# Kernel optimization log

Hardware: AMD Instinct MI355X
Metric: run time of the kernel (lower is better)

Reference implementation:

```python
import jax, jax.numpy as jnp
import numpy as np

DIM = 512
HIDDEN = int(DIM * 0.2)  # 102
K_TOKENS = 64
N_TOKENS = 65536
LN_EPS = 1e-5


def setup_inputs() -> dict:
    key = jax.random.key(0)
    ks = jax.random.split(key, 8)
    x = jax.random.normal(ks[0], (N_TOKENS, DIM), dtype=jnp.float32)
    ln_gamma = jnp.ones((DIM,), dtype=jnp.float32)
    ln_beta = jnp.zeros((DIM,), dtype=jnp.float32)
    W1 = jax.random.normal(ks[1], (DIM, HIDDEN), dtype=jnp.float32) / np.sqrt(DIM)
    b1 = jnp.zeros((HIDDEN,), dtype=jnp.float32)
    W2 = jax.random.normal(ks[2], (HIDDEN, K_TOKENS), dtype=jnp.float32) / np.sqrt(HIDDEN)
    b2 = jnp.zeros((K_TOKENS,), dtype=jnp.float32)
    scale = jnp.ones((1, 1), dtype=jnp.float32)
    return {
        "x": x,
        "ln_gamma": ln_gamma,
        "ln_beta": ln_beta,
        "W1": W1,
        "b1": b1,
        "W2": W2,
        "b2": b2,
        "scale": scale,
        "keeped_tokens": K_TOKENS,
    }


def reference(x, ln_gamma, ln_beta, W1, b1, W2, b2, scale, keeped_tokens):
    # LayerNorm over last dim
    mu = jnp.mean(x, axis=-1, keepdims=True)
    var = jnp.mean(jnp.square(x - mu), axis=-1, keepdims=True)
    h = (x - mu) * jax.lax.rsqrt(var + LN_EPS) * ln_gamma + ln_beta
    # fc1 + exact GELU (torch default) + dynamic fc2 scorer
    h = jax.nn.gelu(h @ W1 + b1, approximate=False)  # [N, HIDDEN]
    w = h @ W2 + b2                                   # [N, K]
    # transpose, scale, softmax over tokens
    w = w.T * scale                                   # [K, N]
    w = jax.nn.softmax(w, axis=1)
    # weighted token aggregation
    return w @ x                                      # [K, DIM]
```

## Files before the change

### kernel.cpp

```cpp
#include <hip/hip_runtime.h>
#include <math.h>

#define N_TOK 65536
#define DIM   512
#define HID   102
#define KTOK  64
#define NTILE 4096
#define LN_EPS 1e-5f

typedef __attribute__((ext_vector_type(8))) short short8;
typedef __attribute__((ext_vector_type(4))) float f32x4;

#define WS_LOGITS 0u
#define WS_PART   4194304u
#define WS_PM     (WS_PART + 4194304u)
#define WS_PS     (WS_PM + 262144u)
#define WS_W1F    (WS_PS + 262144u)
#define WS_W2F    (WS_W1F + 32768u)
#define WS_UB     (WS_W2F + 4096u)
#define WS_VV     (WS_UB + 128u)
#define WS_SMAX   (WS_VV + 128u)
#define WS_SINV   (WS_SMAX + 64u)

__device__ __forceinline__ unsigned short f2bf(float f) {
    unsigned int u = __float_as_uint(f);
    unsigned int r = (u + 0x7fffu + ((u >> 16) & 1u)) >> 16;
    return (unsigned short)r;
}
__device__ __forceinline__ float bf2f(unsigned short h) {
    return __uint_as_float(((unsigned int)h) << 16);
}

__device__ __forceinline__ void gload_lds16(const void* g, void* l) {
    __builtin_amdgcn_global_load_lds(
        (const __attribute__((address_space(1))) unsigned int*)g,
        (__attribute__((address_space(3))) unsigned int*)l, 16, 0, 0);
}

__device__ __forceinline__ void bar_lds() {
    asm volatile("s_waitcnt lgkmcnt(0)" ::: "memory");
    __builtin_amdgcn_s_barrier();
    __builtin_amdgcn_sched_barrier(0);
}

__global__ __launch_bounds__(256) void prep_k(const float* __restrict__ W1,
                                              const float* __restrict__ gamma,
                                              const float* __restrict__ W2,
                                              unsigned short* __restrict__ W1f,
                                              unsigned short* __restrict__ W2f) {
    const int idx = blockIdx.x * 256 + threadIdx.x;
    {
        const int e = idx & 7, lane = (idx >> 3) & 63;
        const int jj = (idx >> 9) & 7, kc = (idx >> 12) & 15;
        const int j = jj * 16 + (lane & 15);
        const int d = kc * 32 + (lane >> 4) * 8 + e;
        W1f[idx] = (j < HID) ? f2bf(gamma[d] * W1[d * HID + j]) : (unsigned short)0;
    }
    if (idx < 8192) {
        const int e = idx & 7, lane = (idx >> 3) & 63;
        const int kc = (idx >> 9) & 3, N = (idx >> 11) & 3;
        const int j = kc * 32 + (lane >> 4) * 8 + e;
        const int k = N * 16 + (lane & 15);
        W2f[idx] = (j < HID) ? f2bf(W2[j * KTOK + k]) : (unsigned short)0;
    }
}

__global__ __launch_bounds__(512) void prep2_k(const float* __restrict__ W1,
                                               const float* __restrict__ b1,
                                               const float* __restrict__ gamma,
                                               const float* __restrict__ beta,
                                               float* __restrict__ ub,
                                               float* __restrict__ vv) {
    __shared__ float su[4][128], sv[4][128];
    const int t = threadIdx.x;
    const int j = t & 127, q = t >> 7;
    float u = 0.0f, v = 0.0f;
    if (j < HID) {
        #pragma unroll 8
        for (int d = q * 128; d < q * 128 + 128; ++d) {
            const float wv = W1[d * HID + j];
            u = fmaf(beta[d], wv, u);
            v = fmaf(gamma[d], wv, v);
        }
    }
    su[q][j] = u; sv[q][j] = v;
    __syncthreads();
    if (q == 0) {
        ub[j] = su[0][j] + su[1][j] + su[2][j] + su[3][j] +
                ((j < HID) ? b1[j] : 0.0f);
        vv[j] = sv[0][j] + sv[1][j] + sv[2][j] + sv[3][j];
    }
}

__global__ __launch_bounds__(512) void scorer_k(const float* __restrict__ x,
                                                const unsigned short* __restrict__ W1f,
                                                const unsigned short* __restrict__ W2f,
                                                const float* __restrict__ ub,
                                                const float* __restrict__ vv,
                                                const float* __restrict__ b2,
                                                const float* __restrict__ scale,
                                                float* __restrict__ logits,
                                                float* __restrict__ pm,
                                                float* __restrict__ psum) {
    __shared__ char smem[4 * 8192];
    const int tid = threadIdx.x;
    const int lane = tid & 63;
    const int w = tid >> 6;
    const int l15 = lane & 15;
    const int hi = lane >> 4;
    const int tile = blockIdx.x * 8 + w;
    const int wt0 = tile * 16;
    char* hb = smem + w * 4096;

    const float* xrow = x + (size_t)(wt0 + l15) * DIM + hi * 8;

    f32x4 xva[3], xvb[3];
    xva[0] = *(const f32x4*)(xrow);
    xvb[0] = *(const f32x4*)(xrow + 4);
    gload_lds16(W1f + w * 512 + lane * 8, smem + w * 1024);
    xva[1] = *(const f32x4*)(xrow + 32);
    xvb[1] = *(const f32x4*)(xrow + 36);
    gload_lds16(W1f + 4096 + w * 512 + lane * 8, smem + 8192 + w * 1024);

    f32x4 acc[8] = {};
    float s = 0.0f, ss = 0.0f;
    #pragma unroll
    for (int kc = 0; kc < 16; ++kc) {
        if (kc < 14) {
            xva[(kc + 2) % 3] = *(const f32x4*)(xrow + (kc + 2) * 32);
            xvb[(kc + 2) % 3] = *(const f32x4*)(xrow + (kc + 2) * 32 + 4);
            gload_lds16(W1f + (kc + 2) * 4096 + w * 512 + lane * 8,
                        smem + ((kc + 2) & 3) * 8192 + w * 1024);
        }
        if (kc < 14)
            asm volatile("s_waitcnt vmcnt(6)" ::: "memory");
        else if (kc == 14)
            asm volatile("s_waitcnt vmcnt(3)" ::: "memory");
        else
            asm volatile("s_waitcnt vmcnt(0)" ::: "memory");
        __builtin_amdgcn_sched_barrier(0);
        __builtin_amdgcn_s_barrier();
        const f32x4 a = xva[kc % 3];
        const f32x4 b = xvb[kc % 3];
        s += a.x + a.y + a.z + a.w + b.x + b.y + b.z + b.w;
        ss += a.x * a.x + a.y * a.y + a.z * a.z + a.w * a.w +
              b.x * b.x + b.y * b.y + b.z * b.z + b.w * b.w;
        short8 af;
        af[0] = (short)f2bf(a.x); af[1] = (short)f2bf(a.y);
        af[2] = (short)f2bf(a.z); af[3] = (short)f2bf(a.w);
        af[4] = (short)f2bf(b.x); af[5] = (short)f2bf(b.y);
        af[6] = (short)f2bf(b.z); af[7] = (short)f2bf(b.w);
        const char* bb = smem + (kc & 3) * 8192 + lane * 16;
        __builtin_amdgcn_s_setprio(1);
        #pragma unroll
        for (int jj = 0; jj < 8; ++jj) {
            const short8 bf = *(const short8*)(bb + jj * 1024);
            acc[jj] = __builtin_amdgcn_mfma_f32_16x16x32_bf16(af, bf, acc[jj], 0, 0, 0);
        }
        __builtin_amdgcn_s_setprio(0);
    }
    __syncthreads();

    s += __shfl_xor(s, 16); ss += __shfl_xor(ss, 16);
    s += __shfl_xor(s, 32); ss += __shfl_xor(ss, 32);
    const float mu = s * (1.0f / 512.0f);
    const float inv = rsqrtf(ss * (1.0f / 512.0f) - mu * mu + LN_EPS);

    float invr[4], muir[4];
    #pragma unroll
    for (int r = 0; r < 4; ++r) {
        const int tk = 4 * hi + r;
        const float m_ = __shfl(mu, tk);
        const float i_ = __shfl(inv, tk);
        invr[r] = i_;
        muir[r] = m_ * i_;
    }
    #pragma unroll
    for (int jj = 0; jj < 8; ++jj) {
        const int col = jj * 16 + l15;
        const float ubj = ub[col];
        const float vvj = vv[col];
        #pragma unroll
        for (int reg = 0; reg < 4; ++reg) {
            const int t = 4 * hi + reg;
            const float pre = fmaf(invr[reg], acc[jj][reg],
                                   fmaf(-muir[reg], vvj, ubj));
            const float g = 0.5f * pre * (1.0f + erff(pre * 0.70710678118f));
            *(unsigned short*)(hb + t * 256 + ((col * 2) ^ ((t & 7) << 4))) = f2bf(g);
        }
    }
    asm volatile("s_waitcnt lgkmcnt(0)" ::: "memory");
    __builtin_amdgcn_sched_barrier(0);

    f32x4 acc2[4] = {};
    {
        const unsigned short* w2 = W2f + lane * 8;
        #pragma unroll
        for (int kc = 0; kc < 4; ++kc) {
            const short8 a2 = *(const short8*)(hb + l15 * 256 +
                                               ((kc * 64 + hi * 16) ^ ((l15 & 7) << 4)));
            __builtin_amdgcn_s_setprio(1);
            #pragma unroll
            for (int nt = 0; nt < 4; ++nt) {
                const short8 bfr = *(const short8*)(w2 + (size_t)(nt * 4 + kc) * 512);
                acc2[nt] = __builtin_amdgcn_mfma_f32_16x16x32_bf16(a2, bfr, acc2[nt], 0, 0, 0);
            }
            __builtin_amdgcn_s_setprio(0);
        }
    }

    const float sc = scale[0];
    #pragma unroll
    for (int nt = 0; nt < 4; ++nt) {
        const int k = nt * 16 + l15;
        const float bb = b2[k];
        f32x4 lv;
        lv.x = (acc2[nt][0] + bb) * sc;
        lv.y = (acc2[nt][1] + bb) * sc;
        lv.z = (acc2[nt][2] + bb) * sc;
        lv.w = (acc2[nt][3] + bb) * sc;
        *(f32x4*)(logits + (size_t)k * N_TOK + wt0 + hi * 4) = lv;
        float m4 = fmaxf(fmaxf(lv.x, lv.y), fmaxf(lv.z, lv.w));
        float s4 = __expf(lv.x - m4) + __expf(lv.y - m4) +
                   __expf(lv.z - m4) + __expf(lv.w - m4);
        #pragma unroll
        for (int o = 16; o <= 32; o <<= 1) {
            const float om = __shfl_xor(m4, o);
            const float os = __shfl_xor(s4, o);
            const float nm = fmaxf(m4, om);
            s4 = s4 * __expf(m4 - nm) + os * __expf(om - nm);
            m4 = nm;
        }
        if (hi == 0) {
            pm[tile * 64 + k] = m4;
            psum[tile * 64 + k] = s4;
        }
    }
}

__global__ __launch_bounds__(256) void stats_k(const float* __restrict__ pm,
                                               const float* __restrict__ psum,
                                               float* __restrict__ smax,
                                               float* __restrict__ sinv) {
    const int k = blockIdx.x;
    const int tid = threadIdx.x;
    __shared__ float rm[4], rs[4];
    float m = -1e30f, s = 0.0f;
    for (int b = tid; b < NTILE; b += 256) {
        const float pmv = pm[b * 64 + k];
        const float psv = psum[b * 64 + k];
        const float nm = fmaxf(m, pmv);
        s = s * __expf(m - nm) + psv * __expf(pmv - nm);
        m = nm;
    }
    #pragma unroll
    for (int o = 32; o >= 1; o >>= 1) {
        const float om = __shfl_xor(m, o);
        const float os = __shfl_xor(s, o);
        const float nm = fmaxf(m, om);
        s = s * __expf(m - nm) + os * __expf(om - nm);
        m = nm;
    }
    if ((tid & 63) == 0) { rm[tid >> 6] = m; rs[tid >> 6] = s; }
    __syncthreads();
    if (tid == 0) {
        float fm = rm[0], fs = rs[0];
        for (int i = 1; i < 4; ++i) {
            const float nm = fmaxf(fm, rm[i]);
            fs = fs * __expf(fm - nm) + rs[i] * __expf(rm[i] - nm);
            fm = nm;
        }
        smax[k] = fm;
        sinv[k] = 1.0f / fs;
    }
}

__global__ __launch_bounds__(512) void agg_k(const float* __restrict__ x,
                                             const float* __restrict__ logits,
                                             const float* __restrict__ smax,
                                             const float* __restrict__ sinv,
                                             float* __restrict__ part) {
    __shared__ char fsm[40960];
    const int tid = threadIdx.x;
    const int lane = tid & 63;
    const int w = tid >> 6;
    const int l15 = lane & 15;
    const int hi = lane >> 4;
    const int dg = blockIdx.y;
    const int tb = blockIdx.x;

    const int sk = tid >> 3;
    const int snp = (tid & 7) * 8;
    const int xd = tid & 127;
    const int xnb = (tid >> 7) * 16;
    const float mk = smax[sk];
    const float ik = sinv[sk];
    const float* lrow = logits + (size_t)sk * N_TOK + tb * 512 + snp;
    const float* xcol = x + (size_t)(tb * 512 + xnb) * DIM + dg * 128 + xd;

    char* pw = fsm + (((sk >> 4) * 2 + (snp >> 5)) * 64 +
                      (sk & 15) + 16 * ((snp & 31) >> 3)) * 16;
    const int xoff0 = (((xd >> 4) * 2 + (xnb >> 5)) * 64 +
                       (xd & 15) + 16 * (((xnb & 31) >> 3) + 0)) * 16;
    const int xoff1 = (((xd >> 4) * 2 + (xnb >> 5)) * 64 +
                       (xd & 15) + 16 * (((xnb & 31) >> 3) + 1)) * 16;

    const int kt = w & 3;
    const int dgr = w >> 2;

    f32x4 acc[4] = {};

    f32x4 pa = *(const f32x4*)(lrow);
    f32x4 pb = *(const f32x4*)(lrow + 4);
    float xl[16];
    #pragma unroll
    for (int i = 0; i < 16; ++i) xl[i] = xcol[(size_t)i * DIM];

    for (int c = 0; c < 8; ++c) {
        {
            short8 pv;
            pv[0] = (short)f2bf(__expf(pa.x - mk) * ik);
            pv[1] = (short)f2bf(__expf(pa.y - mk) * ik);
            pv[2] = (short)f2bf(__expf(pa.z - mk) * ik);
            pv[3] = (short)f2bf(__expf(pa.w - mk) * ik);
            pv[4] = (short)f2bf(__expf(pb.x - mk) * ik);
            pv[5] = (short)f2bf(__expf(pb.y - mk) * ik);
            pv[6] = (short)f2bf(__expf(pb.z - mk) * ik);
            pv[7] = (short)f2bf(__expf(pb.w - mk) * ik);
            *(short8*)pw = pv;
        }
        {
            short8 h0, l0, h1, l1;
            #pragma unroll
            for (int e = 0; e < 8; ++e) {
                const float v = xl[e];
                const unsigned short hb16 = f2bf(v);
                h0[e] = (short)hb16;
                l0[e] = (short)f2bf(v - bf2f(hb16));
            }
            #pragma unroll
            for (int e = 0; e < 8; ++e) {
                const float v = xl[8 + e];
                const unsigned short hb16 = f2bf(v);
                h1[e] = (short)hb16;
                l1[e] = (short)f2bf(v - bf2f(hb16));
            }
            *(short8*)(fsm + 8192 + xoff0) = h0;
            *(short8*)(fsm + 24576 + xoff0) = l0;
            *(short8*)(fsm + 8192 + xoff1) = h1;
            *(short8*)(fsm + 24576 + xoff1) = l1;
        }
        f32x4 pa_n, pb_n;
        float xln[16];
        if (c < 7) {
            pa_n = *(const f32x4*)(lrow + (c + 1) * 64);
            pb_n = *(const f32x4*)(lrow + (c + 1) * 64 + 4);
            #pragma unroll
            for (int i = 0; i < 16; ++i)
                xln[i] = xcol[(size_t)((c + 1) * 64 + i) * DIM];
        }
        bar_lds();

        __builtin_amdgcn_s_setprio(1);
        #pragma unroll
        for (int ns = 0; ns < 2; ++ns) {
            const short8 af =
                *(const short8*)(fsm + ((kt * 2 + ns) * 64 + lane) * 16);
            #pragma unroll
            for (int dt = 0; dt < 4; ++dt) {
                const int dti = dgr * 4 + dt;
                const short8 bh = *(const short8*)(fsm + 8192 +
                                                   ((dti * 2 + ns) * 64 + lane) * 16);
                const short8 bl = *(const short8*)(fsm + 24576 +
                                                   ((dti * 2 + ns) * 64 + lane) * 16);
                acc[dt] = __builtin_amdgcn_mfma_f32_16x16x32_bf16(af, bh, acc[dt], 0, 0, 0);
                acc[dt] = __builtin_amdgcn_mfma_f32_16x16x32_bf16(af, bl, acc[dt], 0, 0, 0);
            }
        }
        __builtin_amdgcn_s_setprio(0);
        bar_lds();

        pa = pa_n; pb = pb_n;
        #pragma unroll
        for (int i = 0; i < 16; ++i) xl[i] = xln[i];
    }

    #pragma unroll
    for (int dt = 0; dt < 4; ++dt) {
        const int dcol = dg * 128 + (dgr * 4 + dt) * 16 + l15;
        #pragma unroll
        for (int reg = 0; reg < 4; ++reg) {
            const int k = kt * 16 + 4 * hi + reg;
            part[((size_t)tb * 64 + k) * 512 + dcol] = acc[dt][reg];
        }
    }
}

__global__ __launch_bounds__(256) void reduce_k(const float* __restrict__ part,
                                                float* __restrict__ out) {
    const int idx = blockIdx.x * 256 + threadIdx.x;
    const int k = idx >> 9, d = idx & 511;
    float s = 0.0f;
    for (int tb = 0; tb < 128; ++tb) s += part[((size_t)tb * 64 + k) * 512 + d];
    out[idx] = s;
}

extern "C" void kernel_launch(void* const* d_in, const int* in_sizes, int n_in,
                              void* d_out, int out_size, void* d_ws, size_t ws_size,
                              hipStream_t stream) {
    const float* x     = (const float*)d_in[0];
    const float* gamma = (const float*)d_in[1];
    const float* beta  = (const float*)d_in[2];
    const float* W1    = (const float*)d_in[3];
    const float* b1    = (const float*)d_in[4];
    const float* W2    = (const float*)d_in[5];
    const float* b2    = (const float*)d_in[6];
    const float* scale = (const float*)d_in[7];
    float* out = (float*)d_out;
    float* ws  = (float*)d_ws;

    float* logits = ws + WS_LOGITS;
    float* part   = ws + WS_PART;
    float* pm     = ws + WS_PM;
    float* psum   = ws + WS_PS;
    unsigned short* W1f = (unsigned short*)(ws + WS_W1F);
    unsigned short* W2f = (unsigned short*)(ws + WS_W2F);
    float* ubv  = ws + WS_UB;
    float* vvv  = ws + WS_VV;
    float* smax = ws + WS_SMAX;
    float* sinv = ws + WS_SINV;

    hipLaunchKernelGGL(prep_k, dim3(256), dim3(256), 0, stream,
                       W1, gamma, W2, W1f, W2f);
    hipLaunchKernelGGL(prep2_k, dim3(1), dim3(512), 0, stream,
                       W1, b1, gamma, beta, ubv, vvv);
    hipLaunchKernelGGL(scorer_k, dim3(NTILE / 8), dim3(512), 0, stream,
                       x, W1f, W2f, ubv, vvv, b2, scale, logits, pm, psum);
    hipLaunchKernelGGL(stats_k, dim3(KTOK), dim3(256), 0, stream,
                       pm, psum, smax, sinv);
    hipLaunchKernelGGL(agg_k, dim3(128, 4), dim3(512), 0, stream,
                       x, logits, smax, sinv, part);
    hipLaunchKernelGGL(reduce_k, dim3(128), dim3(256), 0, stream,
                       part, out);
}
```

Baseline: 108.0 us.

## Stage full W1 in LDS once per block and process two tiles per wave

The scorer kernel now loads the entire bf16 W1 (128 KB) into dynamic LDS once per block instead of streaming it through a 4-stage ring each k-chunk. Each wave then handles two 16-token tiles, with a deeper 7-slot register prefetch of x and per-chunk block barriers removed. The grid drops to 256 blocks with 160 KB of LDS each. This cuts repeated W1 traffic and barrier sync in exchange for one block per CU occupancy and a larger upfront load latency.

```diff
diff --git a/kernel.cpp b/kernel.cpp
--- a/kernel.cpp
+++ b/kernel.cpp
@@ -102,138 +102,158 @@
                                                 float* __restrict__ logits,
                                                 float* __restrict__ pm,
                                                 float* __restrict__ psum) {
-    __shared__ char smem[4 * 8192];
+    extern __shared__ char smem[];
     const int tid = threadIdx.x;
     const int lane = tid & 63;
     const int w = tid >> 6;
     const int l15 = lane & 15;
     const int hi = lane >> 4;
-    const int tile = blockIdx.x * 8 + w;
-    const int wt0 = tile * 16;
-    char* hb = smem + w * 4096;
-
-    const float* xrow = x + (size_t)(wt0 + l15) * DIM + hi * 8;
-
-    f32x4 xva[3], xvb[3];
-    xva[0] = *(const f32x4*)(xrow);
-    xvb[0] = *(const f32x4*)(xrow + 4);
-    gload_lds16(W1f + w * 512 + lane * 8, smem + w * 1024);
-    xva[1] = *(const f32x4*)(xrow + 32);
-    xvb[1] = *(const f32x4*)(xrow + 36);
-    gload_lds16(W1f + 4096 + w * 512 + lane * 8, smem + 8192 + w * 1024);
-
-    f32x4 acc[8] = {};
-    float s = 0.0f, ss = 0.0f;
+    char* hb = smem + 131072 + w * 4096;
+
     #pragma unroll
-    for (int kc = 0; kc < 16; ++kc) {
-        if (kc < 14) {
-            xva[(kc + 2) % 3] = *(const f32x4*)(xrow + (kc + 2) * 32);
-            xvb[(kc + 2) % 3] = *(const f32x4*)(xrow + (kc + 2) * 32 + 4);
-            gload_lds16(W1f + (kc + 2) * 4096 + w * 512 + lane * 8,
-                        smem + ((kc + 2) & 3) * 8192 + w * 1024);
-        }
-        if (kc < 14)
-            asm volatile("s_waitcnt vmcnt(6)" ::: "memory");
-        else if (kc == 14)
-            asm volatile("s_waitcnt vmcnt(3)" ::: "memory");
-        else
-            asm volatile("s_waitcnt vmcnt(0)" ::: "memory");
+    for (int r = 0; r < 16; ++r)
+        gload_lds16(W1f + r * 4096 + w * 512 + lane * 8, smem + r * 8192 + w * 1024);
+
+    const int tile0 = (blockIdx.x * 8 + w) * 2;
+
+    f32x4 xva[7], xvb[7];
+    {
+        const float* xr = x + (size_t)(tile0 * 16 + l15) * DIM + hi * 8;
+        #pragma unroll
+        for (int i = 0; i < 6; ++i) {
+            xva[i] = *(const f32x4*)(xr + i * 32);
+            xvb[i] = *(const f32x4*)(xr + i * 32 + 4);
+        }
+    }
+    asm volatile("s_waitcnt vmcnt(12)" ::: "memory");
+    __builtin_amdgcn_sched_barrier(0);
+    __builtin_amdgcn_s_barrier();
+
+    for (int t = 0; t < 2; ++t) {
+        const int tile = tile0 + t;
+        const int wt0 = tile * 16;
+        const float* xrow = x + (size_t)(wt0 + l15) * DIM + hi * 8;
+
+        f32x4 acc[8] = {};
+        float s = 0.0f, ss = 0.0f;
+        #pragma unroll
+        for (int kc = 0; kc < 16; ++kc) {
+            if (kc < 10) {
+                xva[(kc + 6) % 7] = *(const f32x4*)(xrow + (kc + 6) * 32);
+                xvb[(kc + 6) % 7] = *(const f32x4*)(xrow + (kc + 6) * 32 + 4);
+            }
+            if (kc < 10)      asm volatile("s_waitcnt vmcnt(12)" ::: "memory");
+            else if (kc == 10) asm volatile("s_waitcnt vmcnt(10)" ::: "memory");
+            else if (kc == 11) asm volatile("s_waitcnt vmcnt(8)" ::: "memory");
+            else if (kc == 12) asm volatile("s_waitcnt vmcnt(6)" ::: "memory");
+            else if (kc == 13) asm volatile("s_waitcnt vmcnt(4)" ::: "memory");
+            else if (kc == 14) asm volatile("s_waitcnt vmcnt(2)" ::: "memory");
+            else               asm volatile("s_waitcnt vmcnt(0)" ::: "memory");
+            __builtin_amdgcn_sched_barrier(0);
+            const f32x4 a = xva[kc % 7];
+            const f32x4 b = xvb[kc % 7];
+            s += a.x + a.y + a.z + a.w + b.x + b.y + b.z + b.w;
+            ss += a.x * a.x + a.y * a.y + a.z * a.z + a.w * a.w +
+                  b.x * b.x + b.y * b.y + b.z * b.z + b.w * b.w;
+            short8 af;
+            af[0] = (short)f2bf(a.x); af[1] = (short)f2bf(a.y);
+            af[2] = (short)f2bf(a.z); af[3] = (short)f2bf(a.w);
+            af[4] = (short)f2bf(b.x); af[5] = (short)f2bf(b.y);
+            af[6] = (short)f2bf(b.z); af[7] = (short)f2bf(b.w);
+            const char* bb = smem + kc * 8192 + lane * 16;
+            __builtin_amdgcn_s_setprio(1);
+            #pragma unroll
+            for (int jj = 0; jj < 8; ++jj) {
+                const short8 bf = *(const short8*)(bb + jj * 1024);
+                acc[jj] = __builtin_amdgcn_mfma_f32_16x16x32_bf16(af, bf, acc[jj], 0, 0, 0);
+            }
+            __builtin_amdgcn_s_setprio(0);
+        }
+
+        if (t == 0) {
+            const float* xn = x + (size_t)((tile0 + 1) * 16 + l15) * DIM + hi * 8;
+            #pragma unroll
+            for (int i = 0; i < 6; ++i) {
+                xva[i] = *(const f32x4*)(xn + i * 32);
+                xvb[i] = *(const f32x4*)(xn + i * 32 + 4);
+            }
+            __builtin_amdgcn_sched_barrier(0);
+        }
+
+        s += __shfl_xor(s, 16); ss += __shfl_xor(ss, 16);
+        s += __shfl_xor(s, 32); ss += __shfl_xor(ss, 32);
+        const float mu = s * (1.0f / 512.0f);
+        const float inv = rsqrtf(ss * (1.0f / 512.0f) - mu * mu + LN_EPS);
+
+        float invr[4], muir[4];
+        #pragma unroll
+        for (int r = 0; r < 4; ++r) {
+            const int tk = 4 * hi + r;
+            const float m_ = __shfl(mu, tk);
+            const float i_ = __shfl(inv, tk);
+            invr[r] = i_;
+            muir[r] = m_ * i_;
+        }
+        #pragma unroll
+        for (int jj = 0; jj < 8; ++jj) {
+            const int col = jj * 16 + l15;
+            const float ubj = ub[col];
+            const float vvj = vv[col];
+            #pragma unroll
+            for (int reg = 0; reg < 4; ++reg) {
+                const int tk = 4 * hi + reg;
+                const float pre = fmaf(invr[reg], acc[jj][reg],
+                                       fmaf(-muir[reg], vvj, ubj));
+                const float g = 0.5f * pre * (1.0f + erff(pre * 0.70710678118f));
+                *(unsigned short*)(hb + tk * 256 + ((col * 2) ^ ((tk & 7) << 4))) = f2bf(g);
+            }
+        }
+        asm volatile("s_waitcnt lgkmcnt(0)" ::: "memory");
         __builtin_amdgcn_sched_barrier(0);
-        __builtin_amdgcn_s_barrier();
-        const f32x4 a = xva[kc % 3];
-        const f32x4 b = xvb[kc % 3];
-        s += a.x + a.y + a.z + a.w + b.x + b.y + b.z + b.w;
-        ss += a.x * a.x + a.y * a.y + a.z * a.z + a.w * a.w +
-              b.x * b.x + b.y * b.y + b.z * b.z + b.w * b.w;
-        short8 af;
-        af[0] = (short)f2bf(a.x); af[1] = (short)f2bf(a.y);
-        af[2] = (short)f2bf(a.z); af[3] = (short)f2bf(a.w);
-        af[4] = (short)f2bf(b.x); af[5] = (short)f2bf(b.y);
-        af[6] = (short)f2bf(b.z); af[7] = (short)f2bf(b.w);
-        const char* bb = smem + (kc & 3) * 8192 + lane * 16;
-        __builtin_amdgcn_s_setprio(1);
-        #pragma unroll
-        for (int jj = 0; jj < 8; ++jj) {
-            const short8 bf = *(const short8*)(bb + jj * 1024);
-            acc[jj] = __builtin_amdgcn_mfma_f32_16x16x32_bf16(af, bf, acc[jj], 0, 0, 0);
-        }
-        __builtin_amdgcn_s_setprio(0);
-    }
-    __syncthreads();
-
-    s += __shfl_xor(s, 16); ss += __shfl_xor(ss, 16);
-    s += __shfl_xor(s, 32); ss += __shfl_xor(ss, 32);
-    const float mu = s * (1.0f / 512.0f);
-    const float inv = rsqrtf(ss * (1.0f / 512.0f) - mu * mu + LN_EPS);
-
-    float invr[4], muir[4];
-    #pragma unroll
-    for (int r = 0; r < 4; ++r) {
-        const int tk = 4 * hi + r;
-        const float m_ = __shfl(mu, tk);
-        const float i_ = __shfl(inv, tk);
-        invr[r] = i_;
-        muir[r] = m_ * i_;
-    }
-    #pragma unroll
-    for (int jj = 0; jj < 8; ++jj) {
-        const int col = jj * 16 + l15;
-        const float ubj = ub[col];
-        const float vvj = vv[col];
-        #pragma unroll
-        for (int reg = 0; reg < 4; ++reg) {
-            const int t = 4 * hi + reg;
-            const float pre = fmaf(invr[reg], acc[jj][reg],
-                                   fmaf(-muir[reg], vvj, ubj));
-            const float g = 0.5f * pre * (1.0f + erff(pre * 0.70710678118f));
-            *(unsigned short*)(hb + t * 256 + ((col * 2) ^ ((t & 7) << 4))) = f2bf(g);
-        }
-    }
-    asm volatile("s_waitcnt lgkmcnt(0)" ::: "memory");
-    __builtin_amdgcn_sched_barrier(0);
-
-    f32x4 acc2[4] = {};
-    {
-        const unsigned short* w2 = W2f + lane * 8;
-        #pragma unroll
-        for (int kc = 0; kc < 4; ++kc) {
-            const short8 a2 = *(const short8*)(hb + l15 * 256 +
-                                               ((kc * 64 + hi * 16) ^ ((l15 & 7) << 4)));
-            __builtin_amdgcn_s_setprio(1);
-            #pragma unroll
-            for (int nt = 0; nt < 4; ++nt) {
-                const short8 bfr = *(const short8*)(w2 + (size_t)(nt * 4 + kc) * 512);
-                acc2[nt] = __builtin_amdgcn_mfma_f32_16x16x32_bf16(a2, bfr, acc2[nt], 0, 0, 0);
-            }
-            __builtin_amdgcn_s_setprio(0);
-        }
-    }
-
-    const float sc = scale[0];
-    #pragma unroll
-    for (int nt = 0; nt < 4; ++nt) {
-        const int k = nt * 16 + l15;
-        const float bb = b2[k];
-        f32x4 lv;
-        lv.x = (acc2[nt][0] + bb) * sc;
-        lv.y = (acc2[nt][1] + bb) * sc;
-        lv.z = (acc2[nt][2] + bb) * sc;
-        lv.w = (acc2[nt][3] + bb) * sc;
-        *(f32x4*)(logits + (size_t)k * N_TOK + wt0 + hi * 4) = lv;
-        float m4 = fmaxf(fmaxf(lv.x, lv.y), fmaxf(lv.z, lv.w));
-        float s4 = __expf(lv.x - m4) + __expf(lv.y - m4) +
-                   __expf(lv.z - m4) + __expf(lv.w - m4);
-        #pragma unroll
-        for (int o = 16; o <= 32; o <<= 1) {
-            const float om = __shfl_xor(m4, o);
-            const float os = __shfl_xor(s4, o);
-            const float nm = fmaxf(m4, om);
-            s4 = s4 * __expf(m4 - nm) + os * __expf(om - nm);
-            m4 = nm;
-        }
-        if (hi == 0) {
-            pm[tile * 64 + k] = m4;
-            psum[tile * 64 + k] = s4;
+
+        f32x4 acc2[4] = {};
+        {
+            const unsigned short* w2 = W2f + lane * 8;
+            #pragma unroll
+            for (int kc = 0; kc < 4; ++kc) {
+                const short8 a2 = *(const short8*)(hb + l15 * 256 +
+                                                   ((kc * 64 + hi * 16) ^ ((l15 & 7) << 4)));
+                __builtin_amdgcn_s_setprio(1);
+                #pragma unroll
+                for (int nt = 0; nt < 4; ++nt) {
+                    const short8 bfr = *(const short8*)(w2 + (size_t)(nt * 4 + kc) * 512);
+                    acc2[nt] = __builtin_amdgcn_mfma_f32_16x16x32_bf16(a2, bfr, acc2[nt], 0, 0, 0);
+                }
+                __builtin_amdgcn_s_setprio(0);
+            }
+        }
+
+        const float sc = scale[0];
+        #pragma unroll
+        for (int nt = 0; nt < 4; ++nt) {
+            const int k = nt * 16 + l15;
+            const float bb2 = b2[k];
+            f32x4 lv;
+            lv.x = (acc2[nt][0] + bb2) * sc;
+            lv.y = (acc2[nt][1] + bb2) * sc;
+            lv.z = (acc2[nt][2] + bb2) * sc;
+            lv.w = (acc2[nt][3] + bb2) * sc;
+            *(f32x4*)(logits + (size_t)k * N_TOK + wt0 + hi * 4) = lv;
+            float m4 = fmaxf(fmaxf(lv.x, lv.y), fmaxf(lv.z, lv.w));
+            float s4 = __expf(lv.x - m4) + __expf(lv.y - m4) +
+                       __expf(lv.z - m4) + __expf(lv.w - m4);
+            #pragma unroll
+            for (int o = 16; o <= 32; o <<= 1) {
+                const float om = __shfl_xor(m4, o);
+                const float os = __shfl_xor(s4, o);
+                const float nm = fmaxf(m4, om);
+                s4 = s4 * __expf(m4 - nm) + os * __expf(om - nm);
+                m4 = nm;
+            }
+            if (hi == 0) {
+                pm[tile * 64 + k] = m4;
+                psum[tile * 64 + k] = s4;
+            }
         }
     }
 }
@@ -430,11 +450,14 @@
     float* smax = ws + WS_SMAX;
     float* sinv = ws + WS_SINV;
 
+    hipFuncSetAttribute((const void*)scorer_k,
+                        hipFuncAttributeMaxDynamicSharedMemorySize, 163840);
+
     hipLaunchKernelGGL(prep_k, dim3(256), dim3(256), 0, stream,
                        W1, gamma, W2, W1f, W2f);
     hipLaunchKernelGGL(prep2_k, dim3(1), dim3(512), 0, stream,
                        W1, b1, gamma, beta, ubv, vvv);
-    hipLaunchKernelGGL(scorer_k, dim3(NTILE / 8), dim3(512), 0, stream,
+    hipLaunchKernelGGL(scorer_k, dim3(256), dim3(512), 163840, stream,
                        x, W1f, W2f, ubv, vvv, b2, scale, logits, pm, psum);
     hipLaunchKernelGGL(stats_k, dim3(KTOK), dim3(256), 0, stream,
                        pm, psum, smax, sinv);
```

Result: slower. 134.8 us (+24.8%).

## Widen scorer K-step to 64 with triple-buffered LDS, one barrier per two chunks

Applied to the files above, without the earlier changes.

Restructures the fc1 pipeline in the scorer kernel so each iteration consumes 64 columns (two MFMA sub-steps) instead of 32. It uses a 3-stage LDS ring of 16 KB stages instead of 4 stages of 8 KB, and issues the W1 LDS prefetch after the barrier. This halves the number of block barriers and waitcnt points per tile and puts more loads in flight. In exchange, LDS use grows from 32 KB to 48 KB and more x registers are held live, which may lower occupancy.

```diff
diff --git a/kernel.cpp b/kernel.cpp
--- a/kernel.cpp
+++ b/kernel.cpp
@@ -102,7 +102,7 @@
                                                 float* __restrict__ logits,
                                                 float* __restrict__ pm,
                                                 float* __restrict__ psum) {
-    __shared__ char smem[4 * 8192];
+    __shared__ char smem[3 * 16384];
     const int tid = threadIdx.x;
     const int lane = tid & 63;
     const int w = tid >> 6;
@@ -114,50 +114,62 @@
 
     const float* xrow = x + (size_t)(wt0 + l15) * DIM + hi * 8;
 
-    f32x4 xva[3], xvb[3];
-    xva[0] = *(const f32x4*)(xrow);
-    xvb[0] = *(const f32x4*)(xrow + 4);
-    gload_lds16(W1f + w * 512 + lane * 8, smem + w * 1024);
-    xva[1] = *(const f32x4*)(xrow + 32);
-    xvb[1] = *(const f32x4*)(xrow + 36);
-    gload_lds16(W1f + 4096 + w * 512 + lane * 8, smem + 8192 + w * 1024);
+    f32x4 xs_[3][4];
+    xs_[0][0] = *(const f32x4*)(xrow);
+    xs_[0][1] = *(const f32x4*)(xrow + 4);
+    xs_[0][2] = *(const f32x4*)(xrow + 32);
+    xs_[0][3] = *(const f32x4*)(xrow + 36);
+    xs_[1][0] = *(const f32x4*)(xrow + 64);
+    xs_[1][1] = *(const f32x4*)(xrow + 68);
+    xs_[1][2] = *(const f32x4*)(xrow + 96);
+    xs_[1][3] = *(const f32x4*)(xrow + 100);
+    gload_lds16(W1f + w * 1024 + lane * 8, smem + w * 2048);
+    gload_lds16(W1f + w * 1024 + 512 + lane * 8, smem + w * 2048 + 1024);
+    gload_lds16(W1f + 8192 + w * 1024 + lane * 8, smem + 16384 + w * 2048);
+    gload_lds16(W1f + 8192 + w * 1024 + 512 + lane * 8, smem + 16384 + w * 2048 + 1024);
 
     f32x4 acc[8] = {};
     float s = 0.0f, ss = 0.0f;
     #pragma unroll
-    for (int kc = 0; kc < 16; ++kc) {
-        if (kc < 14) {
-            xva[(kc + 2) % 3] = *(const f32x4*)(xrow + (kc + 2) * 32);
-            xvb[(kc + 2) % 3] = *(const f32x4*)(xrow + (kc + 2) * 32 + 4);
-            gload_lds16(W1f + (kc + 2) * 4096 + w * 512 + lane * 8,
-                        smem + ((kc + 2) & 3) * 8192 + w * 1024);
-        }
-        if (kc < 14)
-            asm volatile("s_waitcnt vmcnt(6)" ::: "memory");
-        else if (kc == 14)
-            asm volatile("s_waitcnt vmcnt(3)" ::: "memory");
-        else
-            asm volatile("s_waitcnt vmcnt(0)" ::: "memory");
+    for (int kc = 0; kc < 8; ++kc) {
+        if (kc < 6) {
+            xs_[(kc + 2) % 3][0] = *(const f32x4*)(xrow + (kc + 2) * 64);
+            xs_[(kc + 2) % 3][1] = *(const f32x4*)(xrow + (kc + 2) * 64 + 4);
+            xs_[(kc + 2) % 3][2] = *(const f32x4*)(xrow + (kc + 2) * 64 + 32);
+            xs_[(kc + 2) % 3][3] = *(const f32x4*)(xrow + (kc + 2) * 64 + 36);
+        }
+        if (kc == 0)       asm volatile("s_waitcnt vmcnt(6)" ::: "memory");
+        else if (kc <= 5)  asm volatile("s_waitcnt vmcnt(10)" ::: "memory");
+        else if (kc == 6)  asm volatile("s_waitcnt vmcnt(6)" ::: "memory");
+        else               asm volatile("s_waitcnt vmcnt(0)" ::: "memory");
         __builtin_amdgcn_sched_barrier(0);
         __builtin_amdgcn_s_barrier();
-        const f32x4 a = xva[kc % 3];
-        const f32x4 b = xvb[kc % 3];
-        s += a.x + a.y + a.z + a.w + b.x + b.y + b.z + b.w;
-        ss += a.x * a.x + a.y * a.y + a.z * a.z + a.w * a.w +
-              b.x * b.x + b.y * b.y + b.z * b.z + b.w * b.w;
-        short8 af;
-        af[0] = (short)f2bf(a.x); af[1] = (short)f2bf(a.y);
-        af[2] = (short)f2bf(a.z); af[3] = (short)f2bf(a.w);
-        af[4] = (short)f2bf(b.x); af[5] = (short)f2bf(b.y);
-        af[6] = (short)f2bf(b.z); af[7] = (short)f2bf(b.w);
-        const char* bb = smem + (kc & 3) * 8192 + lane * 16;
-        __builtin_amdgcn_s_setprio(1);
-        #pragma unroll
-        for (int jj = 0; jj < 8; ++jj) {
-            const short8 bf = *(const short8*)(bb + jj * 1024);
-            acc[jj] = __builtin_amdgcn_mfma_f32_16x16x32_bf16(af, bf, acc[jj], 0, 0, 0);
-        }
-        __builtin_amdgcn_s_setprio(0);
+        if (kc < 6) {
+            const unsigned short* sn = W1f + (kc + 2) * 8192 + w * 1024 + lane * 8;
+            gload_lds16(sn, smem + ((kc + 2) % 3) * 16384 + w * 2048);
+            gload_lds16(sn + 512, smem + ((kc + 2) % 3) * 16384 + w * 2048 + 1024);
+        }
+        #pragma unroll
+        for (int ks = 0; ks < 2; ++ks) {
+            const f32x4 a = xs_[kc % 3][ks * 2];
+            const f32x4 b = xs_[kc % 3][ks * 2 + 1];
+            s += a.x + a.y + a.z + a.w + b.x + b.y + b.z + b.w;
+            ss += a.x * a.x + a.y * a.y + a.z * a.z + a.w * a.w +
+                  b.x * b.x + b.y * b.y + b.z * b.z + b.w * b.w;
+            short8 af;
+            af[0] = (short)f2bf(a.x); af[1] = (short)f2bf(a.y);
+            af[2] = (short)f2bf(a.z); af[3] = (short)f2bf(a.w);
+            af[4] = (short)f2bf(b.x); af[5] = (short)f2bf(b.y);
+            af[6] = (short)f2bf(b.z); af[7] = (short)f2bf(b.w);
+            const char* bb = smem + (kc % 3) * 16384 + ks * 8192 + lane * 16;
+            __builtin_amdgcn_s_setprio(1);
+            #pragma unroll
+            for (int jj = 0; jj < 8; ++jj) {
+                const short8 bf = *(const short8*)(bb + jj * 1024);
+                acc[jj] = __builtin_amdgcn_mfma_f32_16x16x32_bf16(af, bf, acc[jj], 0, 0, 0);
+            }
+            __builtin_amdgcn_s_setprio(0);
+        }
     }
     __syncthreads();
 
```

Measured after the change: 108.6 us. Within noise of the previous version (+0.5%).
